# Performance work log

Hardware: AMD Instinct MI355X
Metric: run time of the kernel (lower is better)

## Reference

```python
import jax, jax.numpy as jnp
import numpy as np
from jax import lax

B, C_IN, C_OUT, K, H, W, NUM = 32, 256, 256, 3, 28, 28, 8


def setup_inputs() -> dict:
    key = jax.random.key(0)
    k1, k2, k3 = jax.random.split(key, 3)
    inputs = jax.random.normal(k1, (B, C_IN, H, W), dtype=jnp.float32)
    inputs_se = jax.random.uniform(k2, (B, NUM), dtype=jnp.float32)
    # weight bank [out*in*k*k, num], init scale sqrt(1/(c*k*k)) as in the module
    scale = np.sqrt(1.0 / (C_IN * K * K)).astype(np.float32)
    weight = jax.random.normal(k3, (C_OUT * C_IN * K * K, NUM), dtype=jnp.float32) * scale
    bias = jnp.zeros((C_OUT,), dtype=jnp.float32)
    return {"inputs": inputs, "inputs_se": inputs_se, "weight": weight, "bias": bias}


def reference(inputs, inputs_se, weight, bias):
    b, c, h, w = inputs.shape
    out_ch = bias.shape[0]
    # per-sample filter generation: [B, num] @ [num, out*in*k*k] -> [B, out, in, k, k]
    wgen = jnp.einsum('bn,on->bo', inputs_se, weight).reshape(b, out_ch, c, K, K)

    def conv_one(x, wk):
        # x: [C,H,W], wk: [O,C,K,K] -> [O,H,W]  (stride 1, padding 1)
        return lax.conv_general_dilated(
            x[None], wk,
            window_strides=(1, 1), padding=[(1, 1), (1, 1)],
            dimension_numbers=('NCHW', 'OIHW', 'NCHW'))[0]

    out = jax.vmap(conv_one)(inputs, wgen)  # [B, O, H, W]
    return out + bias[None, :, None, None]
```

## Files before the change

kernel.cpp:

```cpp
#include <hip/hip_runtime.h>
#include <hip/hip_fp16.h>

#define BB    32
#define CIN   256
#define COUT  256
#define HH    28
#define WW    28
#define NPIX  784
#define KD    2304
#define HP    30
#define WP    30

#define BM    128
#define BN    128
#define NT    7

#define WGEN_ELEMS ((size_t)BB * COUT * KD)
#define XPAD_OFF   (WGEN_ELEMS)

typedef _Float16 f16x8 __attribute__((ext_vector_type(8)));
typedef float    f32x4 __attribute__((ext_vector_type(4)));

static __device__ __forceinline__ ushort f2h_bits(float v) {
    __half h = __float2half(v);
    return *reinterpret_cast<ushort*>(&h);
}

static __device__ __forceinline__ void gll16(const ushort* g, ushort* l) {
    __builtin_amdgcn_global_load_lds(
        (const __attribute__((address_space(1))) unsigned int*)g,
        (__attribute__((address_space(3))) unsigned int*)l, 16, 0, 0);
}

__global__ __launch_bounds__(256) void gen_w(const float* __restrict__ weight,
                                             const float* __restrict__ se,
                                             ushort* __restrict__ wgen) {
    const int o  = blockIdx.x & 255;
    const int bg = blockIdx.x >> 8;
    const int c  = threadIdx.x;

    __shared__ float  se_sh[BB * 8];
    __shared__ ushort w_sh[KD];

    se_sh[c] = se[c];

    float4 wr[18];
    const float4* wp = (const float4*)(weight + (size_t)(o * CIN + c) * 9 * 8);
#pragma unroll
    for (int i = 0; i < 18; ++i) wr[i] = wp[i];
    __syncthreads();

#pragma unroll
    for (int bi = 0; bi < 4; ++bi) {
        const int b = bg * 4 + bi;
        const float s0 = se_sh[b * 8 + 0], s1 = se_sh[b * 8 + 1];
        const float s2 = se_sh[b * 8 + 2], s3 = se_sh[b * 8 + 3];
        const float s4 = se_sh[b * 8 + 4], s5 = se_sh[b * 8 + 5];
        const float s6 = se_sh[b * 8 + 6], s7 = se_sh[b * 8 + 7];
#pragma unroll
        for (int khw = 0; khw < 9; ++khw) {
            const float4 w0 = wr[khw * 2 + 0];
            const float4 w1 = wr[khw * 2 + 1];
            const float v = w0.x * s0 + w0.y * s1 + w0.z * s2 + w0.w * s3
                          + w1.x * s4 + w1.y * s5 + w1.z * s6 + w1.w * s7;
            w_sh[khw * 256 + c] = f2h_bits(v);
        }
        __syncthreads();
        const uint4* src = (const uint4*)w_sh;
        uint4* dst = (uint4*)(wgen + ((size_t)b * COUT + o) * KD);
        dst[c] = src[c];
        if (c < 32) dst[256 + c] = src[256 + c];
        __syncthreads();
    }
}

__global__ __launch_bounds__(256) void gen_x(const float* __restrict__ x,
                                             ushort* __restrict__ xpad) {
    const int bid = blockIdx.x;
    const int hp  = bid % HP;
    const int b   = bid / HP;
    const int tid = threadIdx.x;

    ushort* row = xpad + ((size_t)b * HP + hp) * WP * CIN;

    if (hp == 0 || hp == HP - 1) {
        uint* r32 = (uint*)row;
        for (int i = tid; i < (WP * CIN) / 2; i += 256) r32[i] = 0u;
        return;
    }
    {
        uint* c0 = (uint*)row;
        uint* c1 = (uint*)(row + (WP - 1) * CIN);
        if (tid < 128)       c0[tid] = 0u;
        else                 c1[tid - 128] = 0u;
    }

    __shared__ float lds[CIN * (WW + 1)];
    const int h = hp - 1;
    const float* xr = x + (size_t)b * CIN * NPIX + h * WW;

    for (int f = tid; f < CIN * WW; f += 256) {
        const int c = f / WW;
        const int w = f % WW;
        lds[c * (WW + 1) + w] = xr[(size_t)c * NPIX + w];
    }
    __syncthreads();
    for (int g = tid; g < WW * CIN; g += 256) {
        const int w = g >> 8;
        const int c = g & 255;
        row[(w + 1) * CIN + c] = f2h_bits(lds[c * (WW + 1) + w]);
    }
}

__global__ __launch_bounds__(256) void dconv_mfma(const ushort* __restrict__ wgen,
                                                  const ushort* __restrict__ xpad,
                                                  const float* __restrict__ bias,
                                                  float* __restrict__ out) {
    const int bid   = blockIdx.x;
    const int g     = bid & 7;
    const int s     = bid >> 3;
    const int nt    = s % NT;
    const int slice = g + 8 * (s / NT);
    const int b     = slice >> 1;
    const int mt    = slice & 1;

    const int tid  = threadIdx.x;
    const int lane = tid & 63;
    const int wave = tid >> 6;
    const int wm   = wave >> 1;
    const int wn   = wave & 1;
    const int col  = lane & 15;
    const int quad = lane >> 4;

    __shared__ ushort Ash[2][BM * 32];
    __shared__ ushort Psh[2][4 * 8 * 30 * 8];

    const int mo   = mt * BM + wm * 64;
    const int no   = nt * BN + wn * 64;
    const int h_lo = (nt * BN) / WW;

    const ushort* wg = wgen + ((size_t)b * COUT + mt * BM) * KD;
    const ushort* xp = xpad + (size_t)b * HP * WP * CIN;

    int a_goff[2], a_loff[2];
#pragma unroll
    for (int r = 0; r < 2; ++r) {
        const int cch = r * 256 + tid;
        const int m   = cch >> 2;
        const int kc  = (cch & 3) ^ ((m >> 1) & 3);
        a_goff[r] = m * 9 * CIN + kc * 8;
        a_loff[r] = cch * 8;
    }
    int p_goff[4], p_loff[4];
    bool p_ok[4];
#pragma unroll
    for (int r = 0; r < 4; ++r) {
        const int j = r * 256 + tid;
        p_ok[r] = (j < 960);
        const int jj  = p_ok[r] ? j : 0;
        const int qc  = jj / 240;
        const int rem = jj % 240;
        const int rr  = rem / 30;
        const int ww  = rem % 30;
        int srow = h_lo + rr;
        if (srow > 29) srow = 29;
        p_goff[r] = (srow * WP + ww) * CIN + qc * 8;
        p_loff[r] = jj * 8;
    }

    int pixbase[4], pst[4];
#pragma unroll
    for (int j = 0; j < 4; ++j) {
        const int p  = no + j * 16 + col;
        pst[j] = p;
        const int pc = p > (NPIX - 1) ? (NPIX - 1) : p;
        pixbase[j] = (pc / WW - h_lo) * 30 + (pc % WW);
    }
    const int s_sw  = (col >> 1) & 3;
    const int abase = ((wm * 64 + col) << 2) + (quad ^ s_sw);

    f32x4 acc[4][4];
#pragma unroll
    for (int mi = 0; mi < 4; ++mi)
#pragma unroll
        for (int nj = 0; nj < 4; ++nj)
            acc[mi][nj] = (f32x4){0.f, 0.f, 0.f, 0.f};

#pragma unroll
    for (int r = 0; r < 2; ++r)
        gll16(wg + a_goff[r], &Ash[0][a_loff[r]]);
#pragma unroll
    for (int r = 0; r < 4; ++r)
        if (p_ok[r]) gll16(xp + p_goff[r], &Psh[0][p_loff[r]]);

    for (int step = 0; step < 72; ++step) {
        const int khw  = step % 9;
        const int c32  = step / 9;
        const int abuf = step & 1;
        const int pbuf = c32 & 1;

        __syncthreads();

        if (step + 1 < 72) {
            const int nkhw = (step + 1) % 9;
            const int nc32 = (step + 1) / 9;
            const int aoff = nkhw * 256 + nc32 * 32;
#pragma unroll
            for (int r = 0; r < 2; ++r)
                gll16(wg + a_goff[r] + aoff, &Ash[abuf ^ 1][a_loff[r]]);
            if (nkhw == 0) {
                const int poff = nc32 * 32;
#pragma unroll
                for (int r = 0; r < 4; ++r)
                    if (p_ok[r]) gll16(xp + p_goff[r] + poff,
                                       &Psh[pbuf ^ 1][p_loff[r]]);
            }
        }

        const int koff = (khw / 3) * 30 + (khw % 3);

        f16x8 af[4];
#pragma unroll
        for (int sub = 0; sub < 4; ++sub)
            af[sub] = ((const f16x8*)Ash[abuf])[abase + sub * 64];

        f16x8 bf[4];
#pragma unroll
        for (int j = 0; j < 4; ++j)
            bf[j] = ((const f16x8*)Psh[pbuf])[quad * 240 + pixbase[j] + koff];

#pragma unroll
        for (int mi = 0; mi < 4; ++mi)
#pragma unroll
            for (int nj = 0; nj < 4; ++nj)
                acc[mi][nj] = __builtin_amdgcn_mfma_f32_16x16x32_f16(
                    af[mi], bf[nj], acc[mi][nj], 0, 0, 0);
    }

    float* ob = out + (size_t)b * COUT * NPIX;
#pragma unroll
    for (int mi = 0; mi < 4; ++mi) {
        const int m = mo + mi * 16 + quad * 4;
        const float4 bv = *(const float4*)(bias + m);
#pragma unroll
        for (int nj = 0; nj < 4; ++nj) {
            const int p = pst[nj];
            if (p < NPIX) {
                ob[(size_t)(m + 0) * NPIX + p] = acc[mi][nj][0] + bv.x;
                ob[(size_t)(m + 1) * NPIX + p] = acc[mi][nj][1] + bv.y;
                ob[(size_t)(m + 2) * NPIX + p] = acc[mi][nj][2] + bv.z;
                ob[(size_t)(m + 3) * NPIX + p] = acc[mi][nj][3] + bv.w;
            }
        }
    }
}

extern "C" void kernel_launch(void* const* d_in, const int* in_sizes, int n_in,
                              void* d_out, int out_size, void* d_ws, size_t ws_size,
                              hipStream_t stream) {
    const float* x      = (const float*)d_in[0];
    const float* se     = (const float*)d_in[1];
    const float* weight = (const float*)d_in[2];
    const float* bias   = (const float*)d_in[3];
    float* out          = (float*)d_out;

    ushort* wgen = (ushort*)d_ws;
    ushort* xpad = (ushort*)d_ws + XPAD_OFF;
    (void)ws_size; (void)in_sizes; (void)n_in; (void)out_size;

    gen_w<<<dim3(COUT * 8), dim3(256), 0, stream>>>(weight, se, wgen);
    gen_x<<<dim3(BB * HP), dim3(256), 0, stream>>>(x, xpad);
    dconv_mfma<<<dim3(BB * 2 * NT), dim3(256), 0, stream>>>(wgen, xpad, bias, out);
}
```

Measured before the change: 162.7 us.

## Split-K conv over two channel halves with atomic accumulation and fused prep kernel

Merges the weight-generation and input-padding kernels into one prep kernel, which also pre-fills the output with bias. The conv kernel splits the input-channel reduction in two, doubling the grid, and accumulates partial results with float atomics. It also drops LDS double buffering and issues loads synchronously, adding barriers per step. This targets low occupancy from the small grid and per-launch overhead. The cost is atomic write traffic, an extra full-output bias write, and loss of load/compute overlap.

```diff
diff --git a/kernel.cpp b/kernel.cpp
--- a/kernel.cpp
+++ b/kernel.cpp
@@ -18,6 +18,11 @@
 #define WGEN_ELEMS ((size_t)BB * COUT * KD)
 #define XPAD_OFF   (WGEN_ELEMS)
 
+#define PREP_GENW  2048
+#define PREP_GENX  960
+#define PREP_INIT  448
+#define PREP_GRID  (PREP_GENW + PREP_GENX + PREP_INIT)
+
 typedef _Float16 f16x8 __attribute__((ext_vector_type(8)));
 typedef float    f32x4 __attribute__((ext_vector_type(4)));
 
@@ -32,95 +37,107 @@
         (__attribute__((address_space(3))) unsigned int*)l, 16, 0, 0);
 }
 
-__global__ __launch_bounds__(256) void gen_w(const float* __restrict__ weight,
-                                             const float* __restrict__ se,
-                                             ushort* __restrict__ wgen) {
-    const int o  = blockIdx.x & 255;
-    const int bg = blockIdx.x >> 8;
-    const int c  = threadIdx.x;
-
-    __shared__ float  se_sh[BB * 8];
-    __shared__ ushort w_sh[KD];
-
-    se_sh[c] = se[c];
-
-    float4 wr[18];
-    const float4* wp = (const float4*)(weight + (size_t)(o * CIN + c) * 9 * 8);
-#pragma unroll
-    for (int i = 0; i < 18; ++i) wr[i] = wp[i];
-    __syncthreads();
-
-#pragma unroll
-    for (int bi = 0; bi < 4; ++bi) {
-        const int b = bg * 4 + bi;
-        const float s0 = se_sh[b * 8 + 0], s1 = se_sh[b * 8 + 1];
-        const float s2 = se_sh[b * 8 + 2], s3 = se_sh[b * 8 + 3];
-        const float s4 = se_sh[b * 8 + 4], s5 = se_sh[b * 8 + 5];
-        const float s6 = se_sh[b * 8 + 6], s7 = se_sh[b * 8 + 7];
-#pragma unroll
-        for (int khw = 0; khw < 9; ++khw) {
-            const float4 w0 = wr[khw * 2 + 0];
-            const float4 w1 = wr[khw * 2 + 1];
-            const float v = w0.x * s0 + w0.y * s1 + w0.z * s2 + w0.w * s3
-                          + w1.x * s4 + w1.y * s5 + w1.z * s6 + w1.w * s7;
-            w_sh[khw * 256 + c] = f2h_bits(v);
-        }
+__global__ __launch_bounds__(256) void prep(const float* __restrict__ weight,
+                                            const float* __restrict__ se,
+                                            const float* __restrict__ x,
+                                            const float* __restrict__ bias,
+                                            ushort* __restrict__ wgen,
+                                            ushort* __restrict__ xpad,
+                                            float* __restrict__ out) {
+    __shared__ __align__(16) char smem[29696];
+    const int bid = blockIdx.x;
+    const int tid = threadIdx.x;
+
+    if (bid < PREP_GENW) {
+        const int o  = bid & 255;
+        const int bg = bid >> 8;
+        float*  se_sh = (float*)smem;
+        ushort* w_sh  = (ushort*)(smem + 1024);
+        const int c = tid;
+
+        se_sh[c] = se[c];
+        float4 wr[18];
+        const float4* wp = (const float4*)(weight + (size_t)(o * CIN + c) * 9 * 8);
+#pragma unroll
+        for (int i = 0; i < 18; ++i) wr[i] = wp[i];
         __syncthreads();
-        const uint4* src = (const uint4*)w_sh;
-        uint4* dst = (uint4*)(wgen + ((size_t)b * COUT + o) * KD);
-        dst[c] = src[c];
-        if (c < 32) dst[256 + c] = src[256 + c];
+
+#pragma unroll
+        for (int bi = 0; bi < 4; ++bi) {
+            const int b = bg * 4 + bi;
+            const float s0 = se_sh[b * 8 + 0], s1 = se_sh[b * 8 + 1];
+            const float s2 = se_sh[b * 8 + 2], s3 = se_sh[b * 8 + 3];
+            const float s4 = se_sh[b * 8 + 4], s5 = se_sh[b * 8 + 5];
+            const float s6 = se_sh[b * 8 + 6], s7 = se_sh[b * 8 + 7];
+#pragma unroll
+            for (int khw = 0; khw < 9; ++khw) {
+                const float4 w0 = wr[khw * 2 + 0];
+                const float4 w1 = wr[khw * 2 + 1];
+                const float v = w0.x * s0 + w0.y * s1 + w0.z * s2 + w0.w * s3
+                              + w1.x * s4 + w1.y * s5 + w1.z * s6 + w1.w * s7;
+                w_sh[khw * 256 + c] = f2h_bits(v);
+            }
+            __syncthreads();
+            const uint4* src = (const uint4*)w_sh;
+            uint4* dst = (uint4*)(wgen + ((size_t)b * COUT + o) * KD);
+            dst[c] = src[c];
+            if (c < 32) dst[256 + c] = src[256 + c];
+            __syncthreads();
+        }
+    } else if (bid < PREP_GENW + PREP_GENX) {
+        const int idx = bid - PREP_GENW;
+        const int hp  = idx % HP;
+        const int b   = idx / HP;
+        ushort* row = xpad + ((size_t)b * HP + hp) * WP * CIN;
+
+        if (hp == 0 || hp == HP - 1) {
+            uint* r32 = (uint*)row;
+            for (int i = tid; i < (WP * CIN) / 2; i += 256) r32[i] = 0u;
+            return;
+        }
+        {
+            uint* c0 = (uint*)row;
+            uint* c1 = (uint*)(row + (WP - 1) * CIN);
+            if (tid < 128)       c0[tid] = 0u;
+            else                 c1[tid - 128] = 0u;
+        }
+        float* lds = (float*)smem;
+        const int h = hp - 1;
+        const float* xr = x + (size_t)b * CIN * NPIX + h * WW;
+
+        for (int f = tid; f < CIN * WW; f += 256) {
+            const int c = f / WW;
+            const int w = f % WW;
+            lds[c * (WW + 1) + w] = xr[(size_t)c * NPIX + w];
+        }
         __syncthreads();
-    }
-}
-
-__global__ __launch_bounds__(256) void gen_x(const float* __restrict__ x,
-                                             ushort* __restrict__ xpad) {
-    const int bid = blockIdx.x;
-    const int hp  = bid % HP;
-    const int b   = bid / HP;
-    const int tid = threadIdx.x;
-
-    ushort* row = xpad + ((size_t)b * HP + hp) * WP * CIN;
-
-    if (hp == 0 || hp == HP - 1) {
-        uint* r32 = (uint*)row;
-        for (int i = tid; i < (WP * CIN) / 2; i += 256) r32[i] = 0u;
-        return;
-    }
-    {
-        uint* c0 = (uint*)row;
-        uint* c1 = (uint*)(row + (WP - 1) * CIN);
-        if (tid < 128)       c0[tid] = 0u;
-        else                 c1[tid - 128] = 0u;
-    }
-
-    __shared__ float lds[CIN * (WW + 1)];
-    const int h = hp - 1;
-    const float* xr = x + (size_t)b * CIN * NPIX + h * WW;
-
-    for (int f = tid; f < CIN * WW; f += 256) {
-        const int c = f / WW;
-        const int w = f % WW;
-        lds[c * (WW + 1) + w] = xr[(size_t)c * NPIX + w];
-    }
-    __syncthreads();
-    for (int g = tid; g < WW * CIN; g += 256) {
-        const int w = g >> 8;
-        const int c = g & 255;
-        row[(w + 1) * CIN + c] = f2h_bits(lds[c * (WW + 1) + w]);
+        for (int g2 = tid; g2 < WW * CIN; g2 += 256) {
+            const int w = g2 >> 8;
+            const int c = g2 & 255;
+            row[(w + 1) * CIN + c] = f2h_bits(lds[c * (WW + 1) + w]);
+        }
+    } else {
+        const int idx = bid - PREP_GENW - PREP_GENX;
+        float4* o4 = (float4*)out;
+        const int total4 = BB * COUT * NPIX / 4;
+        for (int i = idx * 256 + tid; i < total4; i += PREP_INIT * 256) {
+            const int o = (i / (NPIX / 4)) & (COUT - 1);
+            const float bv = bias[o];
+            o4[i] = (float4){bv, bv, bv, bv};
+        }
     }
 }
 
 __global__ __launch_bounds__(256) void dconv_mfma(const ushort* __restrict__ wgen,
                                                   const ushort* __restrict__ xpad,
-                                                  const float* __restrict__ bias,
                                                   float* __restrict__ out) {
     const int bid   = blockIdx.x;
     const int g     = bid & 7;
     const int s     = bid >> 3;
-    const int nt    = s % NT;
-    const int slice = g + 8 * (s / NT);
+    const int t     = s % 14;
+    const int nt    = t % 7;
+    const int ks    = t / 7;
+    const int slice = g + 8 * (s / 14);
     const int b     = slice >> 1;
     const int mt    = slice & 1;
 
@@ -132,8 +149,8 @@
     const int col  = lane & 15;
     const int quad = lane >> 4;
 
-    __shared__ ushort Ash[2][BM * 32];
-    __shared__ ushort Psh[2][4 * 8 * 30 * 8];
+    __shared__ ushort Ash[BM * 32];
+    __shared__ ushort Psh[4 * 8 * 30 * 8];
 
     const int mo   = mt * BM + wm * 64;
     const int no   = nt * BN + wn * 64;
@@ -186,70 +203,60 @@
         for (int nj = 0; nj < 4; ++nj)
             acc[mi][nj] = (f32x4){0.f, 0.f, 0.f, 0.f};
 
-#pragma unroll
-    for (int r = 0; r < 2; ++r)
-        gll16(wg + a_goff[r], &Ash[0][a_loff[r]]);
-#pragma unroll
-    for (int r = 0; r < 4; ++r)
-        if (p_ok[r]) gll16(xp + p_goff[r], &Psh[0][p_loff[r]]);
-
-    for (int step = 0; step < 72; ++step) {
-        const int khw  = step % 9;
-        const int c32  = step / 9;
-        const int abuf = step & 1;
-        const int pbuf = c32 & 1;
-
+    for (int cc = 0; cc < 4; ++cc) {
+        const int c32  = ks * 4 + cc;
+        const int coff = c32 * 32;
         __syncthreads();
 
-        if (step + 1 < 72) {
-            const int nkhw = (step + 1) % 9;
-            const int nc32 = (step + 1) / 9;
-            const int aoff = nkhw * 256 + nc32 * 32;
-#pragma unroll
-            for (int r = 0; r < 2; ++r)
-                gll16(wg + a_goff[r] + aoff, &Ash[abuf ^ 1][a_loff[r]]);
-            if (nkhw == 0) {
-                const int poff = nc32 * 32;
-#pragma unroll
-                for (int r = 0; r < 4; ++r)
-                    if (p_ok[r]) gll16(xp + p_goff[r] + poff,
-                                       &Psh[pbuf ^ 1][p_loff[r]]);
+#pragma unroll
+        for (int r = 0; r < 4; ++r)
+            if (p_ok[r]) gll16(xp + p_goff[r] + coff, Psh + p_loff[r]);
+#pragma unroll
+        for (int r = 0; r < 2; ++r)
+            gll16(wg + a_goff[r] + coff, Ash + a_loff[r]);
+
+#pragma unroll
+        for (int khw = 0; khw < 9; ++khw) {
+            if (khw > 0) {
+                __syncthreads();
+#pragma unroll
+                for (int r = 0; r < 2; ++r)
+                    gll16(wg + a_goff[r] + khw * 256 + coff, Ash + a_loff[r]);
             }
-        }
-
-        const int koff = (khw / 3) * 30 + (khw % 3);
-
-        f16x8 af[4];
-#pragma unroll
-        for (int sub = 0; sub < 4; ++sub)
-            af[sub] = ((const f16x8*)Ash[abuf])[abase + sub * 64];
-
-        f16x8 bf[4];
-#pragma unroll
-        for (int j = 0; j < 4; ++j)
-            bf[j] = ((const f16x8*)Psh[pbuf])[quad * 240 + pixbase[j] + koff];
-
-#pragma unroll
-        for (int mi = 0; mi < 4; ++mi)
-#pragma unroll
-            for (int nj = 0; nj < 4; ++nj)
-                acc[mi][nj] = __builtin_amdgcn_mfma_f32_16x16x32_f16(
-                    af[mi], bf[nj], acc[mi][nj], 0, 0, 0);
+            __syncthreads();
+
+            const int koff = (khw / 3) * 30 + (khw % 3);
+
+            f16x8 af[4];
+#pragma unroll
+            for (int sub = 0; sub < 4; ++sub)
+                af[sub] = ((const f16x8*)Ash)[abase + sub * 64];
+
+            f16x8 bf[4];
+#pragma unroll
+            for (int j = 0; j < 4; ++j)
+                bf[j] = ((const f16x8*)Psh)[quad * 240 + pixbase[j] + koff];
+
+#pragma unroll
+            for (int mi = 0; mi < 4; ++mi)
+#pragma unroll
+                for (int nj = 0; nj < 4; ++nj)
+                    acc[mi][nj] = __builtin_amdgcn_mfma_f32_16x16x32_f16(
+                        af[mi], bf[nj], acc[mi][nj], 0, 0, 0);
+        }
     }
 
     float* ob = out + (size_t)b * COUT * NPIX;
 #pragma unroll
     for (int mi = 0; mi < 4; ++mi) {
         const int m = mo + mi * 16 + quad * 4;
-        const float4 bv = *(const float4*)(bias + m);
 #pragma unroll
         for (int nj = 0; nj < 4; ++nj) {
             const int p = pst[nj];
             if (p < NPIX) {
-                ob[(size_t)(m + 0) * NPIX + p] = acc[mi][nj][0] + bv.x;
-                ob[(size_t)(m + 1) * NPIX + p] = acc[mi][nj][1] + bv.y;
-                ob[(size_t)(m + 2) * NPIX + p] = acc[mi][nj][2] + bv.z;
-                ob[(size_t)(m + 3) * NPIX + p] = acc[mi][nj][3] + bv.w;
+#pragma unroll
+                for (int r = 0; r < 4; ++r)
+                    unsafeAtomicAdd(&ob[(size_t)(m + r) * NPIX + p], acc[mi][nj][r]);
             }
         }
     }
@@ -268,7 +275,6 @@
     ushort* xpad = (ushort*)d_ws + XPAD_OFF;
     (void)ws_size; (void)in_sizes; (void)n_in; (void)out_size;
 
-    gen_w<<<dim3(COUT * 8), dim3(256), 0, stream>>>(weight, se, wgen);
-    gen_x<<<dim3(BB * HP), dim3(256), 0, stream>>>(x, xpad);
-    dconv_mfma<<<dim3(BB * 2 * NT), dim3(256), 0, stream>>>(wgen, xpad, bias, out);
-}
+    prep<<<dim3(PREP_GRID), dim3(256), 0, stream>>>(weight, se, x, bias, wgen, xpad, out);
+    dconv_mfma<<<dim3(BB * 2 * NT * 2), dim3(256), 0, stream>>>(wgen, xpad, out);
+}
```

Result: slower. 178.7 us (+9.8%).
